# Kernel tuning notes

Measured on AMD Instinct MI355X. Metric: run time of the kernel, lower is better.

## Reference

```python
import jax, jax.numpy as jnp
import numpy as np

B, N, E, H, AD, V, STEPS = 32, 256, 4, 512, 256, 10000, 5


def setup_inputs() -> dict:
    key = jax.random.key(0)
    ks = jax.random.split(key, 16)
    s = 0.02  # xavier-ish init scale
    return {
        "annotation": jax.random.randint(ks[0], (B, N), 0, V),
        "A": jax.random.normal(ks[1], (B, N, 2 * N * E), dtype=jnp.float32),
        "emb": jax.random.normal(ks[2], (V, AD), dtype=jnp.float32) * s,
        "W_in": jax.random.normal(ks[3], (E, H, H), dtype=jnp.float32) * s,
        "b_in": jnp.zeros((E, H), jnp.float32),
        "W_out": jax.random.normal(ks[4], (E, H, H), dtype=jnp.float32) * s,
        "b_out": jnp.zeros((E, H), jnp.float32),
        "Wr": jax.random.normal(ks[5], (3 * H, H), dtype=jnp.float32) * s,
        "br": jnp.zeros((H,), jnp.float32),
        "Wz": jax.random.normal(ks[6], (3 * H, H), dtype=jnp.float32) * s,
        "bz": jnp.zeros((H,), jnp.float32),
        "Wh": jax.random.normal(ks[7], (3 * H, H), dtype=jnp.float32) * s,
        "bh": jnp.zeros((H,), jnp.float32),
        "Wo": jax.random.normal(ks[8], (H + AD, H), dtype=jnp.float32) * s,
        "bo": jnp.zeros((H,), jnp.float32),
    }


def reference(annotation, A, emb, W_in, b_in, W_out, b_out,
              Wr, br, Wz, bz, Wh, bh, Wo, bo):
    ann = emb[annotation]                                   # [B, N, AD]
    pad = jnp.zeros((B, N, H - AD), ann.dtype)
    prop = jnp.concatenate([ann, pad], axis=2)              # [B, N, H]
    A_in, A_out = A[:, :, :N * E], A[:, :, N * E:]          # [B, N, N*E] each

    for _ in range(STEPS):
        # fused per-edge-type linears: [B, E, N, H] -> [B, E*N, H]
        ins = (jnp.einsum('bnd,edh->benh', prop, W_in)
               + b_in[None, :, None, :]).reshape(B, E * N, H)
        outs = (jnp.einsum('bnd,edh->benh', prop, W_out)
                + b_out[None, :, None, :]).reshape(B, E * N, H)
        a_in = jnp.matmul(A_in, ins)                        # [B, N, H]
        a_out = jnp.matmul(A_out, outs)                     # [B, N, H]
        a = jnp.concatenate([a_in, a_out, prop], axis=2)    # [B, N, 3H]
        r = jax.nn.sigmoid(a @ Wr + br)
        z = jax.nn.sigmoid(a @ Wz + bz)
        j = jnp.concatenate([a_in, a_out, r * prop], axis=2)
        h_hat = jnp.tanh(j @ Wh + bh)
        prop = (1.0 - z) * prop + z * h_hat

    join = jnp.concatenate([prop, ann], axis=2)             # [B, N, H+AD]
    return jnp.tanh(join @ Wo + bo)                         # [B, N, H]
```

## Files before the change

### kernel.cpp

```cpp
#include <hip/hip_runtime.h>
#include <hip/hip_bf16.h>
#include <cstdint>
#include <cstddef>

typedef unsigned short u16;
typedef _Float16 f16;
typedef f16 f16x8 __attribute__((ext_vector_type(8)));
typedef float f32x4 __attribute__((ext_vector_type(4)));

static __device__ __forceinline__ u16 f2h(float f) {
    f16 h = (f16)f;
    return *reinterpret_cast<u16*>(&h);
}
static __device__ __forceinline__ float h2f(u16 u) {
    f16 h = *reinterpret_cast<f16*>(&u);
    return (float)h;
}

#define GLL(g, l) __builtin_amdgcn_global_load_lds(                    \
    (const __attribute__((address_space(1))) void*)(g),                \
    (__attribute__((address_space(3))) void*)(l), 16, 0, 0)

static __device__ __forceinline__ int xcd_swz(int fid, int nwg) {
    const int q = nwg >> 3;
    return (fid & 7) * q + (fid >> 3);
}

#define TDIR (32ull * 512 * 1024)

static __device__ __forceinline__ void stage_tile(const u16* __restrict__ src, int ld,
                                                  u16* lds, int wave, int lane) {
    const int r = lane >> 2;
    const int c = ((lane & 3) << 3) ^ ((r & 3) << 3);
    const u16* g0 = src + (size_t)(wave * 32 + r) * ld + c;
    GLL(g0, lds + wave * 1024);
    GLL(g0 + (size_t)16 * ld, lds + wave * 1024 + 512);
}

static __device__ __forceinline__ void stage_tile64(const u16* __restrict__ src, int ld,
                                                    u16* lds, int t) {
    const int r = t >> 2;
    const int c = ((t & 3) << 3) ^ ((r & 3) << 3);
    GLL(src + (size_t)r * ld + c, lds + ((t >> 6) << 9));
}

static __device__ __forceinline__ void ds_read_frags(const u16* lA, const u16* lB,
                                                     int wq_r, int wq_c, int lr, int ce,
                                                     f16x8 a[4], f16x8 b[4]) {
    #pragma unroll
    for (int i = 0; i < 4; ++i)
        a[i] = *reinterpret_cast<const f16x8*>(&lA[(wq_r + i * 16 + lr) * 32 + ce]);
    #pragma unroll
    for (int j = 0; j < 4; ++j)
        b[j] = *reinterpret_cast<const f16x8*>(&lB[(wq_c + j * 16 + lr) * 32 + ce]);
}

static __device__ __forceinline__ void mfma16(const f16x8 a[4], const f16x8 b[4],
                                              f32x4 acc[4][4]) {
    #pragma unroll
    for (int i = 0; i < 4; ++i)
        #pragma unroll
        for (int j = 0; j < 4; ++j)
            acc[i][j] = __builtin_amdgcn_mfma_f32_16x16x32_f16(a[i], b[j], acc[i][j], 0, 0, 0);
}

#define WAIT_LGKM0 { asm volatile("s_waitcnt lgkmcnt(0)" ::: "memory"); \
                     __builtin_amdgcn_sched_barrier(0); }
#define WAIT_VM(n) { asm volatile("s_waitcnt vmcnt(" #n ")" ::: "memory"); \
                     __builtin_amdgcn_sched_barrier(0); }

static __device__ __forceinline__ void gemm128p(const u16* __restrict__ a1, int lda1, int ka1,
                                                const u16* __restrict__ a2, int lda2,
                                                const u16* __restrict__ bt, int ldb,
                                                int K, int m0, int n0,
                                                u16* sA, u16* sB, f32x4 acc[4][4])
{
    const int t = threadIdx.x, lane = t & 63, wave = t >> 6;
    const int lr = lane & 15, lk = (lane >> 4) << 3;
    const int ce = lk ^ ((lr & 3) << 3);
    const int wq_r = (wave >> 1) << 6, wq_c = (wave & 1) << 6;
    const int nt = K >> 5;

    auto stA = [&](int kt, u16* dst) {
        const int k0 = kt << 5;
        const u16* s; int ld;
        if (k0 < ka1) { s = a1 + (size_t)m0 * lda1 + k0;         ld = lda1; }
        else          { s = a2 + (size_t)m0 * lda2 + (k0 - ka1); ld = lda2; }
        stage_tile(s, ld, dst, wave, lane);
    };
    auto stB = [&](int kt, u16* dst) {
        stage_tile(bt + (size_t)n0 * ldb + (kt << 5), ldb, dst, wave, lane);
    };

    stA(0, sA);        stB(0, sB);
    stA(1, sA + 4096); stB(1, sB + 4096);
    WAIT_VM(4)
    __builtin_amdgcn_s_barrier();

    for (int ti = 0; ti < nt; ti += 2) {
        {
            f16x8 a[4], b[4];
            ds_read_frags(sA, sB, wq_r, wq_c, lr, ce, a, b);
            WAIT_LGKM0
            __builtin_amdgcn_s_barrier();
            const bool pre = (ti + 2) < nt;
            if (pre) { stA(ti + 2, sA); stB(ti + 2, sB); }
            mfma16(a, b, acc);
            if (pre) { WAIT_VM(4) } else { WAIT_VM(0) }
            __builtin_amdgcn_s_barrier();
        }
        {
            f16x8 a[4], b[4];
            ds_read_frags(sA + 4096, sB + 4096, wq_r, wq_c, lr, ce, a, b);
            WAIT_LGKM0
            __builtin_amdgcn_s_barrier();
            const bool pre = (ti + 3) < nt;
            if (pre) { stA(ti + 3, sA + 4096); stB(ti + 3, sB + 4096); }
            mfma16(a, b, acc);
            if (pre) { WAIT_VM(4) } else { WAIT_VM(0) }
            __builtin_amdgcn_s_barrier();
        }
    }
}

static __device__ __forceinline__ void gemm128p64(const u16* __restrict__ a1, int lda1, int ka1,
                                                  const u16* __restrict__ a2, int lda2,
                                                  const u16* __restrict__ bt, int ldb,
                                                  int K, int m0, int n0,
                                                  u16* sA, u16* sB, f32x4 acc[2][4])
{
    const int t = threadIdx.x, lane = t & 63, wave = t >> 6;
    const int lr = lane & 15, lk = (lane >> 4) << 3;
    const int ce = lk ^ ((lr & 3) << 3);
    const int wq_r = wave << 5;
    const int nt = K >> 5;

    auto stA = [&](int kt, u16* dst) {
        const int k0 = kt << 5;
        const u16* s; int ld;
        if (k0 < ka1) { s = a1 + (size_t)m0 * lda1 + k0;         ld = lda1; }
        else          { s = a2 + (size_t)m0 * lda2 + (k0 - ka1); ld = lda2; }
        stage_tile(s, ld, dst, wave, lane);
    };
    auto stB = [&](int kt, u16* dst) {
        stage_tile64(bt + (size_t)n0 * ldb + (kt << 5), ldb, dst, t);
    };
    auto rdfr = [&](const u16* lA, const u16* lB, f16x8 a[2], f16x8 b[4]) {
        #pragma unroll
        for (int i = 0; i < 2; ++i)
            a[i] = *reinterpret_cast<const f16x8*>(&lA[(wq_r + i * 16 + lr) * 32 + ce]);
        #pragma unroll
        for (int j = 0; j < 4; ++j)
            b[j] = *reinterpret_cast<const f16x8*>(&lB[(j * 16 + lr) * 32 + ce]);
    };
    auto mm = [&](const f16x8 a[2], const f16x8 b[4]) {
        #pragma unroll
        for (int i = 0; i < 2; ++i)
            #pragma unroll
            for (int j = 0; j < 4; ++j)
                acc[i][j] = __builtin_amdgcn_mfma_f32_16x16x32_f16(a[i], b[j], acc[i][j], 0, 0, 0);
    };

    stA(0, sA);        stB(0, sB);
    stA(1, sA + 4096); stB(1, sB + 2048);
    WAIT_VM(3)
    __builtin_amdgcn_s_barrier();

    for (int ti = 0; ti < nt; ti += 2) {
        {
            f16x8 a[2], b[4];
            rdfr(sA, sB, a, b);
            WAIT_LGKM0
            __builtin_amdgcn_s_barrier();
            const bool pre = (ti + 2) < nt;
            if (pre) { stA(ti + 2, sA); stB(ti + 2, sB); }
            mm(a, b);
            if (pre) { WAIT_VM(3) } else { WAIT_VM(0) }
            __builtin_amdgcn_s_barrier();
        }
        {
            f16x8 a[2], b[4];
            rdfr(sA + 4096, sB + 2048, a, b);
            WAIT_LGKM0
            __builtin_amdgcn_s_barrier();
            const bool pre = (ti + 3) < nt;
            if (pre) { stA(ti + 3, sA + 4096); stB(ti + 3, sB + 2048); }
            mm(a, b);
            if (pre) { WAIT_VM(3) } else { WAIT_VM(0) }
            __builtin_amdgcn_s_barrier();
        }
    }
}

#define EPI                                         \
    const int lane = threadIdx.x & 63;              \
    const int wave = threadIdx.x >> 6;              \
    const int wq_r = (wave >> 1) << 6;              \
    const int wq_c = (wave & 1) << 6;               \
    const int lr = lane & 15;                       \
    const int l4 = (lane >> 4) << 2;

#define EPI64                                       \
    const int lane = threadIdx.x & 63;              \
    const int wave = threadIdx.x >> 6;              \
    const int wq_r = wave << 5;                     \
    const int lr = lane & 15;                       \
    const int l4 = (lane >> 4) << 2;

__global__ __launch_bounds__(256, 4) void k_proj(const u16* __restrict__ P,
                                                 const u16* __restrict__ Wio,
                                                 const float* __restrict__ b_in,
                                                 const float* __restrict__ b_out,
                                                 u16* __restrict__ T, int K)
{
    __shared__ u16 sA[2 * 4096], sB[2 * 4096];
    const int fid = xcd_swz(blockIdx.x, gridDim.x);
    const int reg = fid >> 8;
    const int inner = fid & 255;
    const int m = ((reg >> 1) << 4) | (inner & 15);
    const int n = ((reg & 1) << 4) | (inner >> 4);
    const int m0 = m << 7, n0 = n << 7;
    f32x4 acc[4][4] = {};
    gemm128p(P, 512, 512, P, 512, Wio, 512, K, m0, n0, sA, sB, acc);
    EPI
    #pragma unroll
    for (int i = 0; i < 4; ++i) {
        const int row = m0 + wq_r + i * 16 + l4;
        const int b = row >> 8, mm = row & 255;
        #pragma unroll
        for (int j = 0; j < 4; ++j) {
            const int col = n0 + wq_c + j * 16 + lr;
            const int dir = col >> 11, eh = col & 2047;
            const float bia = (dir ? b_out : b_in)[eh];
            const int e = eh >> 9, hh = eh & 511;
            ushort4 w4;
            w4.x = f2h(acc[i][j][0] + bia);
            w4.y = f2h(acc[i][j][1] + bia);
            w4.z = f2h(acc[i][j][2] + bia);
            w4.w = f2h(acc[i][j][3] + bia);
            *reinterpret_cast<ushort4*>(&T[(size_t)dir * TDIR + (size_t)b * 512 * 1024
                                           + (size_t)hh * 1024 + e * 256 + mm]) = w4;
        }
    }
}

__global__ __launch_bounds__(256, 4) void k_amat(const u16* __restrict__ A16,
                                                 const u16* __restrict__ T,
                                                 u16* __restrict__ acat)
{
    __shared__ u16 sA[2 * 4096], sB[2 * 4096];
    const int fid = xcd_swz(blockIdx.x, gridDim.x);
    const int n = fid & 3, m = (fid >> 2) & 1, bd = fid >> 3;
    const int b = bd >> 1, dir = bd & 1;
    const int m0 = m << 7, n0 = n << 7;
    const u16* A1 = A16 + (size_t)b * 256 * 2048 + dir * 1024;
    const u16* Bt = T + (size_t)dir * TDIR + (size_t)b * 512 * 1024;
    f32x4 acc[4][4] = {};
    gemm128p(A1, 2048, 1024, A1, 2048, Bt, 1024, 1024, m0, n0, sA, sB, acc);
    EPI
    #pragma unroll
    for (int i = 0; i < 4; ++i) {
        const int row = m0 + wq_r + i * 16 + l4;
        #pragma unroll
        for (int j = 0; j < 4; ++j) {
            const int col = n0 + wq_c + j * 16 + lr;
            #pragma unroll
            for (int v = 0; v < 4; ++v)
                acat[((size_t)b * 256 + row + v) * 1024 + dir * 512 + col] = f2h(acc[i][j][v]);
        }
    }
}

__global__ __launch_bounds__(256, 4) void k_gates(const u16* __restrict__ acat,
                                                  const u16* __restrict__ P,
                                                  const u16* __restrict__ Wrzh,
                                                  const float* __restrict__ br,
                                                  const float* __restrict__ bz,
                                                  u16* __restrict__ rp,
                                                  u16* __restrict__ z16,
                                                  u16* __restrict__ hp16)
{
    __shared__ u16 sA[2 * 4096], sB[2 * 4096];
    const int fid = xcd_swz(blockIdx.x, gridDim.x);
    const int n = fid % 12, m = fid / 12;
    const int m0 = m << 7, n0 = n << 7;
    const int K = (n0 >= 1024) ? 1024 : 1536;
    f32x4 acc[4][4] = {};
    gemm128p(acat, 1024, 1024, P, 512, Wrzh, 1536, K, m0, n0, sA, sB, acc);
    EPI
    #pragma unroll
    for (int i = 0; i < 4; ++i) {
        const int row = m0 + wq_r + i * 16 + l4;
        #pragma unroll
        for (int j = 0; j < 4; ++j) {
            const int col = n0 + wq_c + j * 16 + lr;
            if (col < 512) {
                const float bia = br[col];
                #pragma unroll
                for (int v = 0; v < 4; ++v) {
                    const float s = 1.0f / (1.0f + __expf(-(acc[i][j][v] + bia)));
                    const size_t idx = (size_t)(row + v) * 512 + col;
                    rp[idx] = f2h(s * h2f(P[idx]));
                }
            } else if (col < 1024) {
                const float bia = bz[col - 512];
                #pragma unroll
                for (int v = 0; v < 4; ++v)
                    z16[(size_t)(row + v) * 512 + (col - 512)] =
                        f2h(1.0f / (1.0f + __expf(-(acc[i][j][v] + bia))));
            } else {
                #pragma unroll
                for (int v = 0; v < 4; ++v)
                    hp16[(size_t)(row + v) * 512 + (col - 1024)] = f2h(acc[i][j][v]);
            }
        }
    }
}

__global__ __launch_bounds__(256, 4) void k_hup(const u16* __restrict__ rp,
                                                const u16* __restrict__ WhP,
                                                const float* __restrict__ bh,
                                                const u16* __restrict__ z16,
                                                const u16* __restrict__ hp16,
                                                u16* __restrict__ P)
{
    __shared__ u16 sA[2 * 4096], sB[2 * 2048];
    const int fid = xcd_swz(blockIdx.x, gridDim.x);
    const int n = fid & 7, m = fid >> 3;
    const int m0 = m << 7, n0 = n << 6;
    f32x4 acc[2][4] = {};
    gemm128p64(rp, 512, 512, rp, 512, WhP, 512, 512, m0, n0, sA, sB, acc);
    EPI64
    #pragma unroll
    for (int i = 0; i < 2; ++i) {
        const int row = m0 + wq_r + i * 16 + l4;
        #pragma unroll
        for (int j = 0; j < 4; ++j) {
            const int col = n0 + j * 16 + lr;
            const float bia = bh[col];
            #pragma unroll
            for (int v = 0; v < 4; ++v) {
                const size_t idx = (size_t)(row + v) * 512 + col;
                const float hh = tanhf(h2f(hp16[idx]) + acc[i][j][v] + bia);
                const float zz = h2f(z16[idx]);
                const float pn = (1.0f - zz) * h2f(P[idx]) + zz * hh;
                P[idx] = f2h(pn);
            }
        }
    }
}

__global__ __launch_bounds__(256, 4) void k_final(const u16* __restrict__ P,
                                                  const u16* __restrict__ annf,
                                                  const u16* __restrict__ Wj,
                                                  const float* __restrict__ bo,
                                                  float* __restrict__ out)
{
    __shared__ u16 sA[2 * 4096], sB[2 * 2048];
    const int fid = xcd_swz(blockIdx.x, gridDim.x);
    const int n = fid & 7, m = fid >> 3;
    const int m0 = m << 7, n0 = n << 6;
    f32x4 acc[2][4] = {};
    gemm128p64(P, 512, 512, annf, 256, Wj, 768, 768, m0, n0, sA, sB, acc);
    EPI64
    #pragma unroll
    for (int i = 0; i < 2; ++i) {
        const int row = m0 + wq_r + i * 16 + l4;
        #pragma unroll
        for (int j = 0; j < 4; ++j) {
            const int col = n0 + j * 16 + lr;
            const float bia = bo[col];
            #pragma unroll
            for (int v = 0; v < 4; ++v)
                out[(size_t)(row + v) * 512 + col] = tanhf(acc[i][j][v] + bia);
        }
    }
}

__global__ void s_gather(const int* __restrict__ ann, const float* __restrict__ emb,
                         u16* __restrict__ P, u16* __restrict__ annf)
{
    const int gid = blockIdx.x * 256 + threadIdx.x;
    const int row = gid >> 9, d = gid & 511;
    float v = 0.0f;
    if (d < 256) v = emb[(size_t)ann[row] * 256 + d];
    const u16 h = f2h(v);
    P[gid] = h;
    if (d < 256) annf[((size_t)row << 8) + d] = h;
}

__global__ void s_cvtA(const float* __restrict__ src, u16* __restrict__ dst)
{
    const size_t base = ((size_t)blockIdx.x * 256 + threadIdx.x) * 8;
    float4 f0 = *reinterpret_cast<const float4*>(src + base);
    float4 f1 = *reinterpret_cast<const float4*>(src + base + 4);
    ushort4 p0 = { f2h(f0.x), f2h(f0.y), f2h(f0.z), f2h(f0.w) };
    ushort4 p1 = { f2h(f1.x), f2h(f1.y), f2h(f1.z), f2h(f1.w) };
    *reinterpret_cast<ushort4*>(dst + base)     = p0;
    *reinterpret_cast<ushort4*>(dst + base + 4) = p1;
}

#define NWIO  (4096 * 512)
#define NWRZH (1536 * 1536)
#define NWHP  (512 * 512)
#define NWJ   (512 * 768)
__global__ void s_weights(const float* __restrict__ Wi, const float* __restrict__ Wo,
                          const float* __restrict__ Wr, const float* __restrict__ Wz,
                          const float* __restrict__ Wh, const float* __restrict__ Wj,
                          u16* __restrict__ dWio, u16* __restrict__ dWrzh,
                          u16* __restrict__ dWhP, u16* __restrict__ dWj)
{
    int gid = blockIdx.x * 256 + threadIdx.x;
    if (gid < NWIO) {
        const int nn = gid >> 9, k = gid & 511;
        const int dir = nn >> 11, e = (nn >> 9) & 3, h = nn & 511;
        const float* W = dir ? Wo : Wi;
        dWio[gid] = f2h(W[(size_t)e * 512 * 512 + (size_t)k * 512 + h]);
        return;
    }
    gid -= NWIO;
    if (gid < NWRZH) {
        const int nn = gid / 1536, k = gid - nn * 1536;
        float v;
        if (nn < 512)       v = Wr[(size_t)k * 512 + nn];
        else if (nn < 1024) v = Wz[(size_t)k * 512 + (nn - 512)];
        else                v = (k < 1024) ? Wh[(size_t)k * 512 + (nn - 1024)] : 0.0f;
        dWrzh[gid] = f2h(v);
        return;
    }
    gid -= NWRZH;
    if (gid < NWHP) {
        const int nn = gid >> 9, k = gid & 511;
        dWhP[gid] = f2h(Wh[(size_t)(1024 + k) * 512 + nn]);
        return;
    }
    gid -= NWHP;
    if (gid < NWJ) {
        const int nn = gid / 768, k = gid - nn * 768;
        dWj[gid] = f2h(Wj[(size_t)k * 512 + nn]);
    }
}

extern "C" void kernel_launch(void* const* d_in, const int* in_sizes, int n_in,
                              void* d_out, int out_size, void* d_ws, size_t ws_size,
                              hipStream_t stream) {
    const int*   ann   = (const int*)d_in[0];
    const float* A     = (const float*)d_in[1];
    const float* emb   = (const float*)d_in[2];
    const float* W_in  = (const float*)d_in[3];
    const float* b_in  = (const float*)d_in[4];
    const float* W_out = (const float*)d_in[5];
    const float* b_out = (const float*)d_in[6];
    const float* Wr    = (const float*)d_in[7];
    const float* br    = (const float*)d_in[8];
    const float* Wz    = (const float*)d_in[9];
    const float* bz    = (const float*)d_in[10];
    const float* Wh    = (const float*)d_in[11];
    const float* bh    = (const float*)d_in[12];
    const float* Wo    = (const float*)d_in[13];
    const float* bo    = (const float*)d_in[14];
    float* out = (float*)d_out;

    char* ws = (char*)d_ws;
    size_t off = 0;
    auto alloc = [&](size_t bytes) -> void* {
        void* p = ws + off;
        off = (off + bytes + 255) & ~(size_t)255;
        return p;
    };
    u16* z16   = (u16*)alloc(8192ull * 512 * 2);
    u16* hp16  = (u16*)alloc(8192ull * 512 * 2);
    u16* P     = (u16*)alloc(8192ull * 512 * 2);
    u16* rp    = (u16*)alloc(8192ull * 512 * 2);
    u16* annf  = (u16*)alloc(8192ull * 256 * 2);
    u16* acat  = (u16*)alloc(8192ull * 1024 * 2);
    u16* A16   = (u16*)alloc(8192ull * 2048 * 2);
    u16* T     = (u16*)alloc(2 * TDIR * 2);
    u16* WioT  = (u16*)alloc(4096ull * 512 * 2);
    u16* WrzhT = (u16*)alloc(1536ull * 1536 * 2);
    u16* WhPT  = (u16*)alloc(512ull * 512 * 2);
    u16* WjT   = (u16*)alloc(512ull * 768 * 2);

    s_gather<<<16384, 256, 0, stream>>>(ann, emb, P, annf);
    s_cvtA<<<8192, 256, 0, stream>>>(A, A16);
    const int nw = (NWIO + NWRZH + NWHP + NWJ + 255) / 256;
    s_weights<<<nw, 256, 0, stream>>>(W_in, W_out, Wr, Wz, Wh, Wo,
                                      WioT, WrzhT, WhPT, WjT);

    for (int s = 0; s < 5; ++s) {
        k_proj<<<2048, 256, 0, stream>>>(P, WioT, b_in, b_out, T, s == 0 ? 256 : 512);
        k_amat<<<512, 256, 0, stream>>>(A16, T, acat);
        k_gates<<<768, 256, 0, stream>>>(acat, P, WrzhT, br, bz, rp, z16, hp16);
        k_hup<<<512, 256, 0, stream>>>(rp, WhPT, bh, z16, hp16, P);
    }
    k_final<<<512, 256, 0, stream>>>(P, annf, WjT, bo, out);
}
```

Measured before the change: 815.9 us.

## Switch proj, amat and gates GEMMs to 256x256 tiles with 8-wave blocks

Adds a 256x256 tile GEMM with 512 threads (2x4 waves, each computing 128x64) and moves k_proj, k_amat and k_gates onto it. Grid sizes shrink to 512, 128 and 192 blocks. The larger tiles are meant to raise reuse of each staged operand and cut global and LDS traffic per MFMA. In exchange each block uses 64KB of LDS and many more accumulator registers, and occupancy drops to one block per CU. k_amat gets only 128 blocks and k_gates 192, which may underfill the 256 CUs.

```diff
diff --git a/kernel.cpp b/kernel.cpp
--- a/kernel.cpp
+++ b/kernel.cpp
@@ -27,6 +27,97 @@
 }
 
 #define TDIR (32ull * 512 * 1024)
+
+#define WAIT_LGKM0 { asm volatile("s_waitcnt lgkmcnt(0)" ::: "memory"); \
+                     __builtin_amdgcn_sched_barrier(0); }
+#define WAIT_VM(n) { asm volatile("s_waitcnt vmcnt(" #n ")" ::: "memory"); \
+                     __builtin_amdgcn_sched_barrier(0); }
+
+static __device__ __forceinline__ void stage_tile256(const u16* __restrict__ src, int ld,
+                                                     u16* lds, int t) {
+    const int lane = t & 63, wave = t >> 6;
+    const int r0 = wave * 16 + (lane >> 2);
+    const int c = ((lane & 3) << 3) ^ ((r0 & 3) << 3);
+    GLL(src + (size_t)r0 * ld + c, lds + wave * 512);
+    GLL(src + (size_t)(r0 + 128) * ld + c, lds + 4096 + wave * 512);
+}
+
+static __device__ __forceinline__ void gemm256p(const u16* __restrict__ a1, int lda1, int ka1,
+                                                const u16* __restrict__ a2, int lda2,
+                                                const u16* __restrict__ bt, int ldb,
+                                                int K, int m0, int n0,
+                                                u16* sA, u16* sB, f32x4 acc[8][4])
+{
+    const int t = threadIdx.x, lane = t & 63, wave = t >> 6;
+    const int wm = wave >> 2, wn = wave & 3;
+    const int lr = lane & 15, lk = (lane >> 4) << 3;
+    const int ce = lk ^ ((lr & 3) << 3);
+    const int nt = K >> 5;
+
+    auto stA = [&](int kt, u16* dst) {
+        const int k0 = kt << 5;
+        const u16* s; int ld;
+        if (k0 < ka1) { s = a1 + (size_t)m0 * lda1 + k0;         ld = lda1; }
+        else          { s = a2 + (size_t)m0 * lda2 + (k0 - ka1); ld = lda2; }
+        stage_tile256(s, ld, dst, t);
+    };
+    auto stB = [&](int kt, u16* dst) {
+        stage_tile256(bt + (size_t)n0 * ldb + (kt << 5), ldb, dst, t);
+    };
+    auto rdfr = [&](const u16* lA, const u16* lB, f16x8 a[8], f16x8 b[4]) {
+        #pragma unroll
+        for (int i = 0; i < 8; ++i)
+            a[i] = *reinterpret_cast<const f16x8*>(&lA[(wm * 128 + i * 16 + lr) * 32 + ce]);
+        #pragma unroll
+        for (int j = 0; j < 4; ++j)
+            b[j] = *reinterpret_cast<const f16x8*>(&lB[(wn * 64 + j * 16 + lr) * 32 + ce]);
+    };
+    auto mm = [&](const f16x8 a[8], const f16x8 b[4]) {
+        #pragma unroll
+        for (int i = 0; i < 8; ++i)
+            #pragma unroll
+            for (int j = 0; j < 4; ++j)
+                acc[i][j] = __builtin_amdgcn_mfma_f32_16x16x32_f16(a[i], b[j], acc[i][j], 0, 0, 0);
+    };
+
+    stA(0, sA);        stB(0, sB);
+    stA(1, sA + 8192); stB(1, sB + 8192);
+    WAIT_VM(4)
+    __builtin_amdgcn_s_barrier();
+
+    for (int ti = 0; ti < nt; ti += 2) {
+        {
+            f16x8 a[8], b[4];
+            rdfr(sA, sB, a, b);
+            WAIT_LGKM0
+            __builtin_amdgcn_s_barrier();
+            const bool pre = (ti + 2) < nt;
+            if (pre) { stA(ti + 2, sA); stB(ti + 2, sB); }
+            mm(a, b);
+            if (pre) { WAIT_VM(4) } else { WAIT_VM(0) }
+            __builtin_amdgcn_s_barrier();
+        }
+        {
+            f16x8 a[8], b[4];
+            rdfr(sA + 8192, sB + 8192, a, b);
+            WAIT_LGKM0
+            __builtin_amdgcn_s_barrier();
+            const bool pre = (ti + 3) < nt;
+            if (pre) { stA(ti + 3, sA + 8192); stB(ti + 3, sB + 8192); }
+            mm(a, b);
+            if (pre) { WAIT_VM(4) } else { WAIT_VM(0) }
+            __builtin_amdgcn_s_barrier();
+        }
+    }
+}
+
+#define EPI256                                      \
+    const int lane = threadIdx.x & 63;              \
+    const int wave = threadIdx.x >> 6;              \
+    const int wm = wave >> 2;                       \
+    const int wn = wave & 3;                        \
+    const int lr = lane & 15;                       \
+    const int l4 = (lane >> 4) << 2;
 
 static __device__ __forceinline__ void stage_tile(const u16* __restrict__ src, int ld,
                                                   u16* lds, int wave, int lane) {
@@ -36,7 +127,6 @@
     GLL(g0, lds + wave * 1024);
     GLL(g0 + (size_t)16 * ld, lds + wave * 1024 + 512);
 }
-
 static __device__ __forceinline__ void stage_tile64(const u16* __restrict__ src, int ld,
                                                     u16* lds, int t) {
     const int r = t >> 2;
@@ -44,41 +134,16 @@
     GLL(src + (size_t)r * ld + c, lds + ((t >> 6) << 9));
 }
 
-static __device__ __forceinline__ void ds_read_frags(const u16* lA, const u16* lB,
-                                                     int wq_r, int wq_c, int lr, int ce,
-                                                     f16x8 a[4], f16x8 b[4]) {
-    #pragma unroll
-    for (int i = 0; i < 4; ++i)
-        a[i] = *reinterpret_cast<const f16x8*>(&lA[(wq_r + i * 16 + lr) * 32 + ce]);
-    #pragma unroll
-    for (int j = 0; j < 4; ++j)
-        b[j] = *reinterpret_cast<const f16x8*>(&lB[(wq_c + j * 16 + lr) * 32 + ce]);
-}
-
-static __device__ __forceinline__ void mfma16(const f16x8 a[4], const f16x8 b[4],
-                                              f32x4 acc[4][4]) {
-    #pragma unroll
-    for (int i = 0; i < 4; ++i)
-        #pragma unroll
-        for (int j = 0; j < 4; ++j)
-            acc[i][j] = __builtin_amdgcn_mfma_f32_16x16x32_f16(a[i], b[j], acc[i][j], 0, 0, 0);
-}
-
-#define WAIT_LGKM0 { asm volatile("s_waitcnt lgkmcnt(0)" ::: "memory"); \
-                     __builtin_amdgcn_sched_barrier(0); }
-#define WAIT_VM(n) { asm volatile("s_waitcnt vmcnt(" #n ")" ::: "memory"); \
-                     __builtin_amdgcn_sched_barrier(0); }
-
-static __device__ __forceinline__ void gemm128p(const u16* __restrict__ a1, int lda1, int ka1,
-                                                const u16* __restrict__ a2, int lda2,
-                                                const u16* __restrict__ bt, int ldb,
-                                                int K, int m0, int n0,
-                                                u16* sA, u16* sB, f32x4 acc[4][4])
+static __device__ __forceinline__ void gemm128p64(const u16* __restrict__ a1, int lda1, int ka1,
+                                                  const u16* __restrict__ a2, int lda2,
+                                                  const u16* __restrict__ bt, int ldb,
+                                                  int K, int m0, int n0,
+                                                  u16* sA, u16* sB, f32x4 acc[2][4])
 {
     const int t = threadIdx.x, lane = t & 63, wave = t >> 6;
     const int lr = lane & 15, lk = (lane >> 4) << 3;
     const int ce = lk ^ ((lr & 3) << 3);
-    const int wq_r = (wave >> 1) << 6, wq_c = (wave & 1) << 6;
+    const int wq_r = wave << 5;
     const int nt = K >> 5;
 
     auto stA = [&](int kt, u16* dst) {
@@ -89,60 +154,6 @@
         stage_tile(s, ld, dst, wave, lane);
     };
     auto stB = [&](int kt, u16* dst) {
-        stage_tile(bt + (size_t)n0 * ldb + (kt << 5), ldb, dst, wave, lane);
-    };
-
-    stA(0, sA);        stB(0, sB);
-    stA(1, sA + 4096); stB(1, sB + 4096);
-    WAIT_VM(4)
-    __builtin_amdgcn_s_barrier();
-
-    for (int ti = 0; ti < nt; ti += 2) {
-        {
-            f16x8 a[4], b[4];
-            ds_read_frags(sA, sB, wq_r, wq_c, lr, ce, a, b);
-            WAIT_LGKM0
-            __builtin_amdgcn_s_barrier();
-            const bool pre = (ti + 2) < nt;
-            if (pre) { stA(ti + 2, sA); stB(ti + 2, sB); }
-            mfma16(a, b, acc);
-            if (pre) { WAIT_VM(4) } else { WAIT_VM(0) }
-            __builtin_amdgcn_s_barrier();
-        }
-        {
-            f16x8 a[4], b[4];
-            ds_read_frags(sA + 4096, sB + 4096, wq_r, wq_c, lr, ce, a, b);
-            WAIT_LGKM0
-            __builtin_amdgcn_s_barrier();
-            const bool pre = (ti + 3) < nt;
-            if (pre) { stA(ti + 3, sA + 4096); stB(ti + 3, sB + 4096); }
-            mfma16(a, b, acc);
-            if (pre) { WAIT_VM(4) } else { WAIT_VM(0) }
-            __builtin_amdgcn_s_barrier();
-        }
-    }
-}
-
-static __device__ __forceinline__ void gemm128p64(const u16* __restrict__ a1, int lda1, int ka1,
-                                                  const u16* __restrict__ a2, int lda2,
-                                                  const u16* __restrict__ bt, int ldb,
-                                                  int K, int m0, int n0,
-                                                  u16* sA, u16* sB, f32x4 acc[2][4])
-{
-    const int t = threadIdx.x, lane = t & 63, wave = t >> 6;
-    const int lr = lane & 15, lk = (lane >> 4) << 3;
-    const int ce = lk ^ ((lr & 3) << 3);
-    const int wq_r = wave << 5;
-    const int nt = K >> 5;
-
-    auto stA = [&](int kt, u16* dst) {
-        const int k0 = kt << 5;
-        const u16* s; int ld;
-        if (k0 < ka1) { s = a1 + (size_t)m0 * lda1 + k0;         ld = lda1; }
-        else          { s = a2 + (size_t)m0 * lda2 + (k0 - ka1); ld = lda2; }
-        stage_tile(s, ld, dst, wave, lane);
-    };
-    auto stB = [&](int kt, u16* dst) {
         stage_tile64(bt + (size_t)n0 * ldb + (kt << 5), ldb, dst, t);
     };
     auto rdfr = [&](const u16* lA, const u16* lB, f16x8 a[2], f16x8 b[4]) {
@@ -191,14 +202,6 @@
         }
     }
 }
-
-#define EPI                                         \
-    const int lane = threadIdx.x & 63;              \
-    const int wave = threadIdx.x >> 6;              \
-    const int wq_r = (wave >> 1) << 6;              \
-    const int wq_c = (wave & 1) << 6;               \
-    const int lr = lane & 15;                       \
-    const int l4 = (lane >> 4) << 2;
 
 #define EPI64                                       \
     const int lane = threadIdx.x & 63;              \
@@ -207,29 +210,29 @@
     const int lr = lane & 15;                       \
     const int l4 = (lane >> 4) << 2;
 
-__global__ __launch_bounds__(256, 4) void k_proj(const u16* __restrict__ P,
+__global__ __launch_bounds__(512, 1) void k_proj(const u16* __restrict__ P,
                                                  const u16* __restrict__ Wio,
                                                  const float* __restrict__ b_in,
                                                  const float* __restrict__ b_out,
                                                  u16* __restrict__ T, int K)
 {
-    __shared__ u16 sA[2 * 4096], sB[2 * 4096];
+    __shared__ u16 sA[2 * 8192], sB[2 * 8192];
     const int fid = xcd_swz(blockIdx.x, gridDim.x);
-    const int reg = fid >> 8;
-    const int inner = fid & 255;
-    const int m = ((reg >> 1) << 4) | (inner & 15);
-    const int n = ((reg & 1) << 4) | (inner >> 4);
-    const int m0 = m << 7, n0 = n << 7;
-    f32x4 acc[4][4] = {};
-    gemm128p(P, 512, 512, P, 512, Wio, 512, K, m0, n0, sA, sB, acc);
-    EPI
+    const int reg = fid >> 6;
+    const int inner = fid & 63;
+    const int m = ((reg >> 1) << 3) | (inner & 7);
+    const int n = ((reg & 1) << 3) | (inner >> 3);
+    const int m0 = m << 8, n0 = n << 8;
+    f32x4 acc[8][4] = {};
+    gemm256p(P, 512, 512, P, 512, Wio, 512, K, m0, n0, sA, sB, acc);
+    EPI256
     #pragma unroll
-    for (int i = 0; i < 4; ++i) {
-        const int row = m0 + wq_r + i * 16 + l4;
+    for (int i = 0; i < 8; ++i) {
+        const int row = m0 + wm * 128 + i * 16 + l4;
         const int b = row >> 8, mm = row & 255;
         #pragma unroll
         for (int j = 0; j < 4; ++j) {
-            const int col = n0 + wq_c + j * 16 + lr;
+            const int col = n0 + wn * 64 + j * 16 + lr;
             const int dir = col >> 11, eh = col & 2047;
             const float bia = (dir ? b_out : b_in)[eh];
             const int e = eh >> 9, hh = eh & 511;
@@ -244,26 +247,26 @@
     }
 }
 
-__global__ __launch_bounds__(256, 4) void k_amat(const u16* __restrict__ A16,
+__global__ __launch_bounds__(512, 1) void k_amat(const u16* __restrict__ A16,
                                                  const u16* __restrict__ T,
                                                  u16* __restrict__ acat)
 {
-    __shared__ u16 sA[2 * 4096], sB[2 * 4096];
+    __shared__ u16 sA[2 * 8192], sB[2 * 8192];
     const int fid = xcd_swz(blockIdx.x, gridDim.x);
-    const int n = fid & 3, m = (fid >> 2) & 1, bd = fid >> 3;
+    const int n = fid & 1, bd = fid >> 1;
     const int b = bd >> 1, dir = bd & 1;
-    const int m0 = m << 7, n0 = n << 7;
+    const int n0 = n << 8;
     const u16* A1 = A16 + (size_t)b * 256 * 2048 + dir * 1024;
     const u16* Bt = T + (size_t)dir * TDIR + (size_t)b * 512 * 1024;
-    f32x4 acc[4][4] = {};
-    gemm128p(A1, 2048, 1024, A1, 2048, Bt, 1024, 1024, m0, n0, sA, sB, acc);
-    EPI
+    f32x4 acc[8][4] = {};
+    gemm256p(A1, 2048, 1024, A1, 2048, Bt, 1024, 1024, 0, n0, sA, sB, acc);
+    EPI256
     #pragma unroll
-    for (int i = 0; i < 4; ++i) {
-        const int row = m0 + wq_r + i * 16 + l4;
+    for (int i = 0; i < 8; ++i) {
+        const int row = wm * 128 + i * 16 + l4;
         #pragma unroll
         for (int j = 0; j < 4; ++j) {
-            const int col = n0 + wq_c + j * 16 + lr;
+            const int col = n0 + wn * 64 + j * 16 + lr;
             #pragma unroll
             for (int v = 0; v < 4; ++v)
                 acat[((size_t)b * 256 + row + v) * 1024 + dir * 512 + col] = f2h(acc[i][j][v]);
@@ -271,7 +274,7 @@
     }
 }
 
-__global__ __launch_bounds__(256, 4) void k_gates(const u16* __restrict__ acat,
+__global__ __launch_bounds__(512, 1) void k_gates(const u16* __restrict__ acat,
                                                   const u16* __restrict__ P,
                                                   const u16* __restrict__ Wrzh,
                                                   const float* __restrict__ br,
@@ -280,20 +283,20 @@
                                                   u16* __restrict__ z16,
                                                   u16* __restrict__ hp16)
 {
-    __shared__ u16 sA[2 * 4096], sB[2 * 4096];
+    __shared__ u16 sA[2 * 8192], sB[2 * 8192];
     const int fid = xcd_swz(blockIdx.x, gridDim.x);
-    const int n = fid % 12, m = fid / 12;
-    const int m0 = m << 7, n0 = n << 7;
+    const int n = fid % 6, m = fid / 6;
+    const int m0 = m << 8, n0 = n << 8;
     const int K = (n0 >= 1024) ? 1024 : 1536;
-    f32x4 acc[4][4] = {};
-    gemm128p(acat, 1024, 1024, P, 512, Wrzh, 1536, K, m0, n0, sA, sB, acc);
-    EPI
+    f32x4 acc[8][4] = {};
+    gemm256p(acat, 1024, 1024, P, 512, Wrzh, 1536, K, m0, n0, sA, sB, acc);
+    EPI256
     #pragma unroll
-    for (int i = 0; i < 4; ++i) {
-        const int row = m0 + wq_r + i * 16 + l4;
+    for (int i = 0; i < 8; ++i) {
+        const int row = m0 + wm * 128 + i * 16 + l4;
         #pragma unroll
         for (int j = 0; j < 4; ++j) {
-            const int col = n0 + wq_c + j * 16 + lr;
+            const int col = n0 + wn * 64 + j * 16 + lr;
             if (col < 512) {
                 const float bia = br[col];
                 #pragma unroll
@@ -488,9 +491,9 @@
                                       WioT, WrzhT, WhPT, WjT);
 
     for (int s = 0; s < 5; ++s) {
-        k_proj<<<2048, 256, 0, stream>>>(P, WioT, b_in, b_out, T, s == 0 ? 256 : 512);
-        k_amat<<<512, 256, 0, stream>>>(A16, T, acat);
-        k_gates<<<768, 256, 0, stream>>>(acat, P, WrzhT, br, bz, rp, z16, hp16);
+        k_proj<<<512, 512, 0, stream>>>(P, WioT, b_in, b_out, T, s == 0 ? 256 : 512);
+        k_amat<<<128, 512, 0, stream>>>(A16, T, acat);
+        k_gates<<<192, 512, 0, stream>>>(acat, P, WrzhT, br, bz, rp, z16, hp16);
         k_hup<<<512, 256, 0, stream>>>(rp, WhPT, bh, z16, hp16, P);
     }
     k_final<<<512, 256, 0, stream>>>(P, annf, WjT, bo, out);
```

After: 953.5 us. +16.9%, slower.
